# Kernel optimization log

Measured on AMD Instinct MI355X. Metric: run time of the kernel, lower is better.

The kernel has to match this reference:

```python
import jax, jax.numpy as jnp
import numpy as np

HEADS = 4
DIM_K = 16
DIM_U = 1
EPS = 1e-5


def _rel_pos_idx(n):
    # torch: meshgrid(ij) -> stack -> '(i j) n'; rel = pos[None,:]-pos[:,None] + n-1
    ii, jj = np.meshgrid(np.arange(n), np.arange(n), indexing='ij')
    pos = np.stack([ii, jj]).reshape(2, -1).T  # (n*n, 2)
    rel = pos[None, :] - pos[:, None] + (n - 1)  # (N, N, 2)
    return rel[..., 0], rel[..., 1]


def _bn(t, gamma, beta):
    # BatchNorm2d in training mode: batch stats over (b, h, w), biased var
    mu = t.mean(axis=(0, 1, 2))
    var = t.var(axis=(0, 1, 2))
    return (t - mu) * jax.lax.rsqrt(var + EPS) * gamma + beta


def setup_inputs() -> dict:
    key = jax.random.key(0)
    ks = jax.random.split(key, 16)
    b, n, c = 8, 48, 128
    hk = DIM_K * HEADS          # 64
    v = 128 // HEADS            # 32 (dim_out // heads)
    rl = 2 * n - 1              # 95
    s = 0.02
    return {
        'x': jax.random.normal(ks[0], (b, n, n, c), jnp.float32),
        'cor': jax.random.normal(ks[1], (b, n, n, 2), jnp.float32),
        'Wq': jax.random.normal(ks[2], (hk, c), jnp.float32) * s,
        'Wk': jax.random.normal(ks[3], (DIM_K * DIM_U, c), jnp.float32) * s,
        'Wv': jax.random.normal(ks[4], (v * DIM_U, c), jnp.float32) * s,
        'Wce': jax.random.normal(ks[5], (hk, 2), jnp.float32) * s,
        'bce': jax.random.normal(ks[6], (hk,), jnp.float32) * s,
        'Wcc': jax.random.normal(ks[7], (hk, 128), jnp.float32) * s,
        'Wmp': jax.random.normal(ks[8], (128, hk), jnp.float32) * s,
        'bmp': jax.random.normal(ks[9], (128,), jnp.float32) * s,
        'gq': jnp.ones((hk,), jnp.float32),
        'bq': jnp.zeros((hk,), jnp.float32),
        'gv': jnp.ones((v * DIM_U,), jnp.float32),
        'bv': jnp.zeros((v * DIM_U,), jnp.float32),
        'rel_pos_emb': jax.random.normal(ks[10], (rl, rl, DIM_K, DIM_U), jnp.float32),
    }


def reference(x, cor, Wq, Wk, Wv, Wce, bce, Wcc, Wmp, bmp, gq, bq, gv, bv, rel_pos_emb):
    b, hh, ww, c = x.shape
    h, u, kd = HEADS, DIM_U, DIM_K
    vd = Wv.shape[0] // u
    N = hh * ww

    # frame reversal along batch
    x_rev = jnp.concatenate([x[b // 2:], x[:b // 2]], axis=0)

    # 1x1 convs as channel matmuls (channels-last)
    q = jnp.einsum('bhwc,oc->bhwo', x, Wq)
    k = jnp.einsum('bhwc,oc->bhwo', x_rev, Wk)
    v = jnp.einsum('bhwc,oc->bhwo', x_rev, Wv)

    Qn = _bn(q, gq, bq)
    Vn = _bn(v, gv, bv)

    Q = jnp.transpose(Qn.reshape(b, N, h, kd), (0, 2, 3, 1))       # b h k n
    K = jnp.transpose(k.reshape(b, N, u, kd), (0, 2, 3, 1))        # b u k m
    V = jnp.transpose(Vn.reshape(b, N, u, vd), (0, 2, 3, 1))       # b u v m

    K = jax.nn.softmax(K, axis=-1)
    lamc = jnp.einsum('bukm,buvm->bkv', K, V)
    Yc = jnp.einsum('bhkn,bkv->bhvn', Q, lamc)

    # relative position lambda (global branch)
    ni, mi = _rel_pos_idx(hh)
    emb = rel_pos_emb[ni, mi]                                      # n m k u
    lamp = jnp.einsum('nmku,buvm->bnkv', emb, V)
    Yp = jnp.einsum('bhkn,bnkv->bhvn', Q, lamp)

    Y = Yc + Yp                                                    # b h v n
    appearance = jnp.transpose(Y.reshape(b, h, vd, hh, ww), (0, 3, 4, 1, 2)).reshape(b, hh, ww, h * vd)

    cor_embed_ = jnp.einsum('bhwc,oc->bhwo', cor, Wce) + bce       # b hh ww (h k)
    cor_embed = jnp.transpose(cor_embed_.reshape(b, N, h, kd), (0, 2, 3, 1))  # b h k n
    crc = jnp.einsum('bhkn,bkv->bhvn', cor_embed, lamc)
    crp = jnp.einsum('bhkn,bnkv->bhvn', cor_embed, lamp)
    cor_reverse_ = jnp.transpose((crc + crp).reshape(b, h, vd, hh, ww), (0, 3, 4, 1, 2)).reshape(b, hh, ww, h * vd)
    cor_reverse = jnp.einsum('bhwc,oc->bhwo', cor_reverse_, Wcc)
    motion = jnp.einsum('bhwc,oc->bhwo', cor_reverse - cor_embed_, Wmp) + bmp
    return appearance, motion
```

## Files before the change

### kernel.cpp

```cpp
#include <hip/hip_runtime.h>
#include <math.h>

#define NNPOS 2304
#define ROWS  18432
#define NK    96

#define O_Q   0ul
#define O_K   1179648ul
#define O_V   1474560ul
#define O_ST  2064384ul
#define O_VP  2064704ul
#define O_QP  2457920ul
#define O_CE  4817216ul
#define O_LC  5996864ul
#define O_CR  6000960ul
#define O_RT  8360256ul
#define O_WF  8433984ul
#define O_WG  8450368ul
#define O_B2  8450624ul
#define O_WB  8450752ul

typedef __bf16 bf16x8 __attribute__((ext_vector_type(8)));
typedef float  f32x4  __attribute__((ext_vector_type(4)));
typedef unsigned int u32;
typedef u32 u32x4 __attribute__((ext_vector_type(4)));

__device__ inline float wred(float v) {
#pragma unroll
  for (int off = 32; off > 0; off >>= 1) v += __shfl_down(v, off, 64);
  return v;
}

__global__ void k_fold(const float* __restrict__ Wcc, const float* __restrict__ Wce,
                       const float* __restrict__ Wmp, const float* __restrict__ bmp,
                       const float* __restrict__ bce, const float* __restrict__ Wq,
                       const float* __restrict__ Wk, const float* __restrict__ Wv,
                       float* __restrict__ ws) {
  const int t = threadIdx.x;
  const int g = blockIdx.x * 256 + t;
  const int o2 = g >> 7, c = g & 127;
  float acc = 0.f;
#pragma unroll 8
  for (int o = 0; o < 64; ++o) acc += Wmp[o2 * 64 + o] * Wcc[o * 128 + c];
  ws[O_WF + (size_t)c * 128 + o2] = acc;
  if (blockIdx.x == 0 && t < 128) {
    float a0 = 0.f, a1 = 0.f, ab = 0.f;
#pragma unroll 8
    for (int o = 0; o < 64; ++o) {
      float w = Wmp[t * 64 + o];
      a0 += w * Wce[o * 2]; a1 += w * Wce[o * 2 + 1]; ab += w * bce[o];
    }
    ws[O_WG + t * 2] = a0; ws[O_WG + t * 2 + 1] = a1; ws[O_B2 + t] = bmp[t] - ab;
  }
  __bf16* wbp = (__bf16*)(ws + O_WB);
  if (g < 14336) {
    float w;
    if (g < 8192) w = Wq[g];
    else if (g < 10240) w = Wk[g - 8192];
    else w = Wv[g - 10240];
    wbp[g] = (__bf16)w;
  }
}

__global__ __launch_bounds__(256) void k_qkv(const float* __restrict__ x,
                                             float* __restrict__ ws) {
  const int t = threadIdx.x;
  const int wave = t >> 6, lane = t & 63;
  const int lr = lane & 15, quad = lane >> 4;
  const int r0 = blockIdx.x * 64 + wave * 16;
  const int b = r0 / NNPOS;
  const int n0 = r0 - b * NNPOS;
  const size_t outbase = (size_t)(((b + 4) & 7)) * NNPOS + n0;

  const __bf16* wb = (const __bf16*)(ws + O_WB);
  const float* xrow = x + (size_t)(r0 + lr) * 128;

  f32x4 acc[7];
#pragma unroll
  for (int i = 0; i < 7; ++i) acc[i] = (f32x4){0.f, 0.f, 0.f, 0.f};

#pragma unroll
  for (int ks = 0; ks < 4; ++ks) {
    const float* ap = xrow + ks * 32 + quad * 8;
    float4 a0 = *(const float4*)(ap);
    float4 a1 = *(const float4*)(ap + 4);
    bf16x8 af;
    af[0] = (__bf16)a0.x; af[1] = (__bf16)a0.y; af[2] = (__bf16)a0.z; af[3] = (__bf16)a0.w;
    af[4] = (__bf16)a1.x; af[5] = (__bf16)a1.y; af[6] = (__bf16)a1.z; af[7] = (__bf16)a1.w;
#pragma unroll
    for (int ct = 0; ct < 7; ++ct) {
      bf16x8 bfrag = *(const bf16x8*)(wb + (ct * 16 + lr) * 128 + ks * 32 + quad * 8);
      acc[ct] = __builtin_amdgcn_mfma_f32_16x16x32_bf16(af, bfrag, acc[ct], 0, 0, 0);
    }
  }

#pragma unroll
  for (int ct = 0; ct < 7; ++ct) {
#pragma unroll
    for (int reg = 0; reg < 4; ++reg) {
      int m = quad * 4 + reg;
      int oc = ct * 16 + lr;
      float vvv = acc[ct][reg];
      if (ct < 4)      ws[O_Q + (size_t)(r0 + m) * 64 + oc] = vvv;
      else if (ct < 5) ws[O_K + (outbase + m) * 16 + (oc - 64)] = vvv;
      else             ws[O_V + (outbase + m) * 32 + (oc - 80)] = vvv;
    }
  }
}

__global__ void k_rt(const float* __restrict__ rel, float* __restrict__ ws) {
  __bf16* rt = (__bf16*)(ws + O_RT);
  int i = blockIdx.x * 256 + threadIdx.x;
  if (i < 144400) {
    int kc = i & 15, rr = i >> 4;
    int ri = rr / 95, rj = rr - ri * 95;
    rt[(size_t)kc * 9216 + ri * 96 + rj] = (__bf16)rel[i];
  }
}

__global__ void k_zero(float* __restrict__ ws) {
  __bf16* vp = (__bf16*)(ws + O_VP);
  int i = blockIdx.x * 256 + threadIdx.x;
  int bv = i / 96, rem = i - bv * 96;
  int mi = rem >> 1, h8 = rem & 1;
  uint4 z; z.x = 0; z.y = 0; z.z = 0; z.w = 0;
  *(uint4*)(vp + (size_t)bv * 3072 + mi * 64 + 48 + h8 * 8) = z;
}

__global__ void k_stats(const float* __restrict__ gq, const float* __restrict__ bq,
                        const float* __restrict__ gv, const float* __restrict__ bv,
                        float* __restrict__ ws) {
  const int t = threadIdx.x, blk = blockIdx.x;
  const int wave = t >> 6, lane = t & 63;
  __shared__ float r1[4], r2[4];
  if (blk < 96) {
    const bool isq = blk < 64;
    const int ch = isq ? blk : blk - 64;
    const float* src = ws + (isq ? O_Q : O_V);
    const int stride = isq ? 64 : 32;
    float s = 0.f, s2 = 0.f;
    for (int r = t; r < ROWS; r += 256) {
      float v = src[(size_t)r * stride + ch];
      s += v; s2 += v * v;
    }
    s = wred(s); s2 = wred(s2);
    if (lane == 0) { r1[wave] = s; r2[wave] = s2; }
    __syncthreads();
    if (t == 0) {
      float S = r1[0] + r1[1] + r1[2] + r1[3];
      float S2 = r2[0] + r2[1] + r2[2] + r2[3];
      float mu = S / 18432.f;
      float var = S2 / 18432.f - mu * mu;
      float g = isq ? gq[ch] : gv[ch];
      float be = isq ? bq[ch] : bv[ch];
      float sc = g * rsqrtf(var + 1e-5f);
      if (isq) { ws[O_ST + ch] = sc;       ws[O_ST + 64 + ch] = be - mu * sc; }
      else     { ws[O_ST + 128 + ch] = sc; ws[O_ST + 160 + ch] = be - mu * sc; }
    }
  } else {
    const int idx = blk - 96;
    const int b = idx >> 4, kc = idx & 15;
    float s = 0.f;
    for (int m = t; m < NNPOS; m += 256)
      s += __expf(ws[O_K + (size_t)(b * NNPOS + m) * 16 + kc]);
    s = wred(s);
    if (lane == 0) r1[wave] = s;
    __syncthreads();
    if (t == 0) ws[O_ST + 192 + idx] = 1.f / (r1[0] + r1[1] + r1[2] + r1[3]);
  }
}

__global__ void k_prep(const float* __restrict__ cor, const float* __restrict__ Wce,
                       const float* __restrict__ bce, float* __restrict__ ws) {
  const int t = threadIdx.x;
  const int rl = t >> 5, j = t & 31;
  const int rid = blockIdx.x * 8 + rl;
  const int b = rid / NNPOS, n = rid - b * NNPOS;
  const float* st = ws + O_ST;
  __bf16* vp = (__bf16*)(ws + O_VP);
  float vvn = ws[O_V + (size_t)rid * 32 + j] * st[128 + j] + st[160 + j];
  vp[(size_t)(b * 32 + j) * 3072 + (n / 48) * 64 + (n % 48)] = (__bf16)vvn;
  float c0 = cor[rid * 2], c1 = cor[rid * 2 + 1];
#pragma unroll
  for (int ch = j; ch < 64; ch += 32) {
    float qn = ws[O_Q + (size_t)rid * 64 + ch] * st[ch] + st[64 + ch];
    ws[O_QP + (size_t)(n * 8 + b) * 128 + ch] = qn;
    float ce = c0 * Wce[ch * 2] + c1 * Wce[ch * 2 + 1] + bce[ch];
    ws[O_QP + (size_t)(n * 8 + b) * 128 + 64 + ch] = ce;
    ws[O_CE + (size_t)rid * 64 + ch] = ce;
  }
}

__global__ void k_lamc(float* __restrict__ ws) {
  const int b = blockIdx.x >> 4, kc = blockIdx.x & 15;
  const int v = threadIdx.x & 31, chunk = threadIdx.x >> 5;
  const float* st = ws + O_ST;
  const float sc = st[128 + v], bi = st[160 + v];
  float acc = 0.f;
  const int mbeg = chunk * 288;
  for (int m = mbeg; m < mbeg + 288; ++m) {
    float ek = __expf(ws[O_K + (size_t)(b * NNPOS + m) * 16 + kc]);
    float vn = ws[O_V + (size_t)(b * NNPOS + m) * 32 + v] * sc + bi;
    acc += ek * vn;
  }
  __shared__ float red[8][32];
  red[chunk][v] = acc;
  __syncthreads();
  if (chunk == 0) {
    float s = 0.f;
#pragma unroll
    for (int q = 0; q < 8; ++q) s += red[q][v];
    ws[O_LC + (size_t)(b * 16 + kc) * 32 + v] = s * st[192 + b * 16 + kc];
  }
}

__global__ __launch_bounds__(256, 2) void k_lamp(float* __restrict__ ws,
                                                 float* __restrict__ out) {
  __shared__ __align__(16) char smem[33792];
  bf16x8* Bs16 = (bf16x8*)smem;
  u32* Sw = (u32*)(smem + 8192);
  float* Cs = (float*)smem;

  const int t = threadIdx.x;
  const int bx = blockIdx.x;
  const int ni = bx / 6;
  const int sset = bx - ni * 6;
  const int s0 = (sset < 3) ? sset * 16 : (sset - 3) * 16 + 1;
  const int chalf = blockIdx.y;
  const int colbase = chalf * 128;
  const int wave = t >> 6, lane = t & 63;
  const int wrow = wave >> 1, wcol = wave & 1;
  const int lr = lane & 15, quad = lane >> 4;

  const __bf16* vp = (const __bf16*)(ws + O_VP);
  const unsigned short* rp = (const unsigned short*)(ws + O_RT);

  const int ia0 = t;
  const int kcA0 = ia0 / 24, wpA0 = ia0 - kcA0 * 24;
  const int ia1 = t + 256;
  const int kcA1 = ia1 / 24, wpA1 = ia1 - kcA1 * 24;
  const bool hasA1 = (ia1 < 384);

  const int colB0 = t >> 2, pB0 = ((t & 3) - ((t >> 3) & 3)) & 3;
  const int ub1 = t + 256;
  const int colB1 = ub1 >> 2, pB1 = ((ub1 & 3) - ((ub1 >> 3) & 3)) & 3;
  const __bf16* gB0 = vp + (size_t)(colbase + colB0) * 3072 + pB0 * 8;
  const __bf16* gB1 = vp + (size_t)(colbase + colB1) * 3072 + pB1 * 8;

  f32x4 acc[4][4];
  {
    f32x4 zz = {0.f, 0.f, 0.f, 0.f};
#pragma unroll
    for (int i = 0; i < 4; ++i)
#pragma unroll
      for (int j = 0; j < 4; ++j) acc[i][j] = zz;
  }

  u32 sa0 = 0, sa1 = 0;
  bf16x8 vb0, vb1;

  {
    const int P0 = 96 * (47 - ni) - s0 + 33;
    long b0 = (long)kcA0 * 9216 + P0 + 2 * wpA0;
    if (P0 & 1) sa0 = (u32)rp[b0] | ((u32)rp[b0 + 1] << 16);
    else        sa0 = *(const u32*)(rp + b0);
    if (hasA1) {
      long b1 = (long)kcA1 * 9216 + P0 + 2 * wpA1;
      if (P0 & 1) sa1 = (u32)rp[b1] | ((u32)rp[b1 + 1] << 16);
      else        sa1 = *(const u32*)(rp + b1);
    }
    vb0 = *(const bf16x8*)(gB0);
    vb1 = *(const bf16x8*)(gB1);
  }

  for (int ks = 0; ks < NK; ++ks) {
    __syncthreads();
    Sw[kcA0 * 25 + wpA0] = sa0;
    if (hasA1) Sw[kcA1 * 25 + wpA1] = sa1;
    Bs16[t] = vb0;
    Bs16[t + 256] = vb1;
    __syncthreads();

    if (ks < NK - 1) {
      const int ksn = ks + 1;
      const int mi = ksn >> 1, mj0 = (ksn & 1) << 5;
      const int P0 = 96 * (mi - ni + 47) + mj0 - s0 + 33;
      const int k0 = ksn * 32;
      long b0 = (long)kcA0 * 9216 + P0 + 2 * wpA0;
      if (P0 & 1) sa0 = (u32)rp[b0] | ((u32)rp[b0 + 1] << 16);
      else        sa0 = *(const u32*)(rp + b0);
      if (hasA1) {
        long b1 = (long)kcA1 * 9216 + P0 + 2 * wpA1;
        if (P0 & 1) sa1 = (u32)rp[b1] | ((u32)rp[b1 + 1] << 16);
        else        sa1 = *(const u32*)(rp + b1);
      }
      vb0 = *(const bf16x8*)(gB0 + k0);
      vb1 = *(const bf16x8*)(gB1 + k0);
    }

    bf16x8 af[4], bfr[4];
#pragma unroll
    for (int rt = 0; rt < 4; ++rt) {
      int nl = wrow * 4 + rt;
      int wb = lr * 25 + (7 - nl) + quad * 4;
      u32x4 dd = { Sw[wb], Sw[wb + 1], Sw[wb + 2], Sw[wb + 3] };
      af[rt] = __builtin_bit_cast(bf16x8, dd);
    }
#pragma unroll
    for (int ct = 0; ct < 4; ++ct) {
      int col = wcol * 64 + ct * 16 + lr;
      int u = col * 4 + ((quad + (col >> 1)) & 3);
      bfr[ct] = Bs16[u];
    }
#pragma unroll
    for (int rt = 0; rt < 4; ++rt)
#pragma unroll
      for (int ct = 0; ct < 4; ++ct)
        acc[rt][ct] = __builtin_amdgcn_mfma_f32_16x16x32_bf16(af[rt], bfr[ct], acc[rt][ct], 0, 0, 0);
  }

  const float* lamc = ws + O_LC;
  const float* Qp = ws + O_QP;
  float* CR = ws + O_CR;
  const int s = t >> 5, vv = t & 31;

  for (int h = 0; h < 2; ++h) {
    __syncthreads();
    if (wrow == h) {
#pragma unroll
      for (int rt = 0; rt < 4; ++rt) {
#pragma unroll
        for (int ct = 0; ct < 4; ++ct) {
          int col = wcol * 64 + ct * 16 + lr;
          int bb = chalf * 4 + (col >> 5);
          int vl = col & 31;
#pragma unroll
          for (int reg = 0; reg < 4; ++reg) {
            int row = rt * 16 + quad * 4 + reg;
            int kc = row & 15;
            Cs[row * 132 + col] = acc[rt][ct][reg] + lamc[(bb * 16 + kc) * 32 + vl];
          }
        }
      }
    }
    __syncthreads();
#pragma unroll
    for (int i = 0; i < 16; ++i) {
      int combo = s * 16 + i;
      int hp = combo & 7, bl = (combo >> 3) & 3, nr = combo >> 5;
      int n = ni * 48 + s0 + 2 * (h * 4 + nr);
      int bb = chalf * 4 + bl;
      const float* qrow = Qp + ((size_t)(n * 8 + bb) * 8 + hp) * 16;
      const float* crow = Cs + (nr * 16) * 132 + bl * 32 + vv;
      float y = 0.f;
#pragma unroll
      for (int kc = 0; kc < 16; ++kc) y += qrow[kc] * crow[kc * 132];
      float* dst = (hp < 4) ? out : CR;
      dst[(size_t)(bb * NNPOS + n) * 128 + (hp & 3) * 32 + vv] = y;
    }
  }
}

__global__ void k_motion(const float* __restrict__ cor, float* __restrict__ ws,
                         float* __restrict__ out) {
  __shared__ float cr[16][128];
  __shared__ float cc[16][2];
  const int t = threadIdx.x;
  const int r0 = blockIdx.x * 16;
  for (int i = t; i < 2048; i += 256) cr[i >> 7][i & 127] = ws[O_CR + (size_t)r0 * 128 + i];
  if (t < 32) cc[t >> 1][t & 1] = cor[r0 * 2 + t];
  __syncthreads();
  const int o2 = t & 127, rg = t >> 7;
  const float* wft = ws + O_WF;
  float wg0 = ws[O_WG + o2 * 2], wg1 = ws[O_WG + o2 * 2 + 1], b2 = ws[O_B2 + o2];
  float acc[8];
#pragma unroll
  for (int j = 0; j < 8; ++j) {
    int row = rg + 2 * j;
    acc[j] = b2 - cc[row][0] * wg0 - cc[row][1] * wg1;
  }
  for (int c = 0; c < 128; ++c) {
    float w = wft[c * 128 + o2];
#pragma unroll
    for (int j = 0; j < 8; ++j) acc[j] += cr[rg + 2 * j][c] * w;
  }
#pragma unroll
  for (int j = 0; j < 8; ++j)
    out[2359296ul + (size_t)(r0 + rg + 2 * j) * 128 + o2] = acc[j];
}

extern "C" void kernel_launch(void* const* d_in, const int* in_sizes, int n_in,
                              void* d_out, int out_size, void* d_ws, size_t ws_size,
                              hipStream_t stream) {
  const float* x   = (const float*)d_in[0];
  const float* cor = (const float*)d_in[1];
  const float* Wq  = (const float*)d_in[2];
  const float* Wk  = (const float*)d_in[3];
  const float* Wv  = (const float*)d_in[4];
  const float* Wce = (const float*)d_in[5];
  const float* bce = (const float*)d_in[6];
  const float* Wcc = (const float*)d_in[7];
  const float* Wmp = (const float*)d_in[8];
  const float* bmp = (const float*)d_in[9];
  const float* gq  = (const float*)d_in[10];
  const float* bq  = (const float*)d_in[11];
  const float* gv  = (const float*)d_in[12];
  const float* bv  = (const float*)d_in[13];
  const float* rel = (const float*)d_in[14];
  float* out = (float*)d_out;
  float* ws  = (float*)d_ws;

  k_fold  <<<64, 256, 0, stream>>>(Wcc, Wce, Wmp, bmp, bce, Wq, Wk, Wv, ws);
  k_qkv   <<<288, 256, 0, stream>>>(x, ws);
  k_rt    <<<565, 256, 0, stream>>>(rel, ws);
  k_zero  <<<96, 256, 0, stream>>>(ws);
  k_stats <<<224, 256, 0, stream>>>(gq, bq, gv, bv, ws);
  k_prep  <<<2304, 256, 0, stream>>>(cor, Wce, bce, ws);
  k_lamc  <<<128, 256, 0, stream>>>(ws);
  k_lamp  <<<dim3(288, 2), 256, 0, stream>>>(ws, out);
  k_motion<<<1152, 256, 0, stream>>>(cor, ws, out);
}
```

Baseline: 267.7 us.

## Use MFMA for motion GEMM, split stats reductions, double-buffer lamp loads

The motion projection now runs as a bf16 MFMA GEMM, with the folded weight and the cor_reverse intermediate stored in bf16, replacing the scalar fp32 loop. The BN and softmax-sum statistics become a two-stage reduction: many coalesced partial-sum blocks, then one finalizing block. k_lamc is tiled through shared memory and accumulates with atomics, with the softmax normalization deferred to k_lamp. k_lamp's global loads are double-buffered two steps ahead, and the redundant CE store is dropped. The bf16 intermediates lower precision, and the extra launch and atomics add a little overhead.

```diff
diff --git a/kernel.cpp b/kernel.cpp
--- a/kernel.cpp
+++ b/kernel.cpp
@@ -15,21 +15,18 @@
 #define O_LC  5996864ul
 #define O_CR  6000960ul
 #define O_RT  8360256ul
-#define O_WF  8433984ul
 #define O_WG  8450368ul
 #define O_B2  8450624ul
 #define O_WB  8450752ul
+#define O_PT  8457920ul
+#define O_PV  8466112ul
+#define O_PE  8468160ul
+#define O_WFB 8469184ul
 
 typedef __bf16 bf16x8 __attribute__((ext_vector_type(8)));
 typedef float  f32x4  __attribute__((ext_vector_type(4)));
 typedef unsigned int u32;
 typedef u32 u32x4 __attribute__((ext_vector_type(4)));
-
-__device__ inline float wred(float v) {
-#pragma unroll
-  for (int off = 32; off > 0; off >>= 1) v += __shfl_down(v, off, 64);
-  return v;
-}
 
 __global__ void k_fold(const float* __restrict__ Wcc, const float* __restrict__ Wce,
                        const float* __restrict__ Wmp, const float* __restrict__ bmp,
@@ -42,7 +39,7 @@
   float acc = 0.f;
 #pragma unroll 8
   for (int o = 0; o < 64; ++o) acc += Wmp[o2 * 64 + o] * Wcc[o * 128 + c];
-  ws[O_WF + (size_t)c * 128 + o2] = acc;
+  ((__bf16*)(ws + O_WFB))[o2 * 128 + c] = (__bf16)acc;
   if (blockIdx.x == 0 && t < 128) {
     float a0 = 0.f, a1 = 0.f, ab = 0.f;
 #pragma unroll 8
@@ -121,52 +118,95 @@
 __global__ void k_zero(float* __restrict__ ws) {
   __bf16* vp = (__bf16*)(ws + O_VP);
   int i = blockIdx.x * 256 + threadIdx.x;
+  if (i < 4096) ws[O_LC + i] = 0.f;
   int bv = i / 96, rem = i - bv * 96;
   int mi = rem >> 1, h8 = rem & 1;
   uint4 z; z.x = 0; z.y = 0; z.z = 0; z.w = 0;
   *(uint4*)(vp + (size_t)bv * 3072 + mi * 64 + 48 + h8 * 8) = z;
 }
 
-__global__ void k_stats(const float* __restrict__ gq, const float* __restrict__ bq,
-                        const float* __restrict__ gv, const float* __restrict__ bv,
-                        float* __restrict__ ws) {
+__global__ void k_stats1(float* __restrict__ ws) {
   const int t = threadIdx.x, blk = blockIdx.x;
-  const int wave = t >> 6, lane = t & 63;
-  __shared__ float r1[4], r2[4];
-  if (blk < 96) {
-    const bool isq = blk < 64;
-    const int ch = isq ? blk : blk - 64;
-    const float* src = ws + (isq ? O_Q : O_V);
-    const int stride = isq ? 64 : 32;
+  __shared__ float sh[512];
+  if (blk < 64) {
+    const int ch = t & 63, rsub = t >> 6;
+    const float* src = ws + O_Q;
+    const int r0 = blk * 288;
     float s = 0.f, s2 = 0.f;
-    for (int r = t; r < ROWS; r += 256) {
-      float v = src[(size_t)r * stride + ch];
+#pragma unroll 4
+    for (int i = 0; i < 72; ++i) {
+      float v = src[(size_t)(r0 + rsub + i * 4) * 64 + ch];
       s += v; s2 += v * v;
     }
-    s = wred(s); s2 = wred(s2);
-    if (lane == 0) { r1[wave] = s; r2[wave] = s2; }
-    __syncthreads();
-    if (t == 0) {
-      float S = r1[0] + r1[1] + r1[2] + r1[3];
-      float S2 = r2[0] + r2[1] + r2[2] + r2[3];
-      float mu = S / 18432.f;
-      float var = S2 / 18432.f - mu * mu;
-      float g = isq ? gq[ch] : gv[ch];
-      float be = isq ? bq[ch] : bv[ch];
-      float sc = g * rsqrtf(var + 1e-5f);
-      if (isq) { ws[O_ST + ch] = sc;       ws[O_ST + 64 + ch] = be - mu * sc; }
-      else     { ws[O_ST + 128 + ch] = sc; ws[O_ST + 160 + ch] = be - mu * sc; }
+    sh[t] = s; sh[256 + t] = s2;
+    __syncthreads();
+    if (t < 64) {
+      float S = sh[t] + sh[t + 64] + sh[t + 128] + sh[t + 192];
+      float S2 = sh[256 + t] + sh[256 + t + 64] + sh[256 + t + 128] + sh[256 + t + 192];
+      ws[O_PT + blk * 128 + t * 2] = S; ws[O_PT + blk * 128 + t * 2 + 1] = S2;
+    }
+  } else if (blk < 96) {
+    const int j = blk - 64;
+    const int ch = t & 31, rsub = t >> 5;
+    const float* src = ws + O_V;
+    const int r0 = j * 576;
+    float s = 0.f, s2 = 0.f;
+#pragma unroll 4
+    for (int i = 0; i < 72; ++i) {
+      float v = src[(size_t)(r0 + rsub + i * 8) * 32 + ch];
+      s += v; s2 += v * v;
+    }
+    sh[t] = s; sh[256 + t] = s2;
+    __syncthreads();
+    if (t < 32) {
+      float S = 0.f, S2 = 0.f;
+#pragma unroll
+      for (int k = 0; k < 8; ++k) { S += sh[t + k * 32]; S2 += sh[256 + t + k * 32]; }
+      ws[O_PV + j * 64 + t * 2] = S; ws[O_PV + j * 64 + t * 2 + 1] = S2;
     }
   } else {
     const int idx = blk - 96;
-    const int b = idx >> 4, kc = idx & 15;
+    const int b = idx >> 3, sl = idx & 7;
+    const int kc = t & 15, rsub = t >> 4;
+    const int r0 = b * 2304 + sl * 288;
     float s = 0.f;
-    for (int m = t; m < NNPOS; m += 256)
-      s += __expf(ws[O_K + (size_t)(b * NNPOS + m) * 16 + kc]);
-    s = wred(s);
-    if (lane == 0) r1[wave] = s;
-    __syncthreads();
-    if (t == 0) ws[O_ST + 192 + idx] = 1.f / (r1[0] + r1[1] + r1[2] + r1[3]);
+#pragma unroll 2
+    for (int i = 0; i < 18; ++i)
+      s += __expf(ws[O_K + (size_t)(r0 + rsub + i * 16) * 16 + kc]);
+    sh[t] = s;
+    __syncthreads();
+    if (t < 16) {
+      float S = 0.f;
+#pragma unroll
+      for (int k = 0; k < 16; ++k) S += sh[t + k * 16];
+      ws[O_PE + b * 128 + sl * 16 + t] = S;
+    }
+  }
+}
+
+__global__ void k_stats2(const float* __restrict__ gq, const float* __restrict__ bq,
+                         const float* __restrict__ gv, const float* __restrict__ bv,
+                         float* __restrict__ ws) {
+  const int t = threadIdx.x;
+  if (t < 64) {
+    float S = 0.f, S2 = 0.f;
+    for (int i = 0; i < 64; ++i) { S += ws[O_PT + i * 128 + t * 2]; S2 += ws[O_PT + i * 128 + t * 2 + 1]; }
+    float mu = S / 18432.f, var = S2 / 18432.f - mu * mu;
+    float sc = gq[t] * rsqrtf(var + 1e-5f);
+    ws[O_ST + t] = sc; ws[O_ST + 64 + t] = bq[t] - mu * sc;
+  } else if (t < 96) {
+    int ch = t - 64;
+    float S = 0.f, S2 = 0.f;
+    for (int i = 0; i < 32; ++i) { S += ws[O_PV + i * 64 + ch * 2]; S2 += ws[O_PV + i * 64 + ch * 2 + 1]; }
+    float mu = S / 18432.f, var = S2 / 18432.f - mu * mu;
+    float sc = gv[ch] * rsqrtf(var + 1e-5f);
+    ws[O_ST + 128 + ch] = sc; ws[O_ST + 160 + ch] = bv[ch] - mu * sc;
+  } else if (t < 224) {
+    int idx = t - 96; int b = idx >> 4, kc = idx & 15;
+    float S = 0.f;
+#pragma unroll
+    for (int sl = 0; sl < 8; ++sl) S += ws[O_PE + b * 128 + sl * 16 + kc];
+    ws[O_ST + 192 + idx] = 1.f / S;
   }
 }
 
@@ -187,31 +227,37 @@
     ws[O_QP + (size_t)(n * 8 + b) * 128 + ch] = qn;
     float ce = c0 * Wce[ch * 2] + c1 * Wce[ch * 2 + 1] + bce[ch];
     ws[O_QP + (size_t)(n * 8 + b) * 128 + 64 + ch] = ce;
-    ws[O_CE + (size_t)rid * 64 + ch] = ce;
   }
 }
 
 __global__ void k_lamc(float* __restrict__ ws) {
-  const int b = blockIdx.x >> 4, kc = blockIdx.x & 15;
-  const int v = threadIdx.x & 31, chunk = threadIdx.x >> 5;
+  const int b = blockIdx.x / 9, sl = blockIdx.x - b * 9;
+  const int t = threadIdx.x;
+  __shared__ float eK[16][16];
+  __shared__ float Vn[16][33];
   const float* st = ws + O_ST;
-  const float sc = st[128 + v], bi = st[160 + v];
-  float acc = 0.f;
-  const int mbeg = chunk * 288;
-  for (int m = mbeg; m < mbeg + 288; ++m) {
-    float ek = __expf(ws[O_K + (size_t)(b * NNPOS + m) * 16 + kc]);
-    float vn = ws[O_V + (size_t)(b * NNPOS + m) * 32 + v] * sc + bi;
-    acc += ek * vn;
-  }
-  __shared__ float red[8][32];
-  red[chunk][v] = acc;
-  __syncthreads();
-  if (chunk == 0) {
-    float s = 0.f;
-#pragma unroll
-    for (int q = 0; q < 8; ++q) s += red[q][v];
-    ws[O_LC + (size_t)(b * 16 + kc) * 32 + v] = s * st[192 + b * 16 + kc];
-  }
+  const int kc = t & 15, vp_ = t >> 4;
+  const int v0 = vp_ * 2, v1 = v0 + 1;
+  float a0 = 0.f, a1 = 0.f;
+  const int m0 = b * 2304 + sl * 256;
+  const int jj = t & 31, rw = t >> 5;
+  const float scj = st[128 + jj], bij = st[160 + jj];
+  for (int ch = 0; ch < 16; ++ch) {
+    const int mbase = m0 + ch * 16;
+    eK[t >> 4][t & 15] = __expf(ws[O_K + (size_t)(mbase + (t >> 4)) * 16 + (t & 15)]);
+    Vn[rw][jj]     = ws[O_V + (size_t)(mbase + rw) * 32 + jj] * scj + bij;
+    Vn[rw + 8][jj] = ws[O_V + (size_t)(mbase + rw + 8) * 32 + jj] * scj + bij;
+    __syncthreads();
+#pragma unroll
+    for (int m = 0; m < 16; ++m) {
+      float e = eK[m][kc];
+      a0 += e * Vn[m][v0];
+      a1 += e * Vn[m][v1];
+    }
+    __syncthreads();
+  }
+  atomicAdd(&ws[O_LC + (size_t)(b * 16 + kc) * 32 + v0], a0);
+  atomicAdd(&ws[O_LC + (size_t)(b * 16 + kc) * 32 + v1], a1);
 }
 
 __global__ __launch_bounds__(256, 2) void k_lamp(float* __restrict__ ws,
@@ -256,47 +302,36 @@
       for (int j = 0; j < 4; ++j) acc[i][j] = zz;
   }
 
-  u32 sa0 = 0, sa1 = 0;
-  bf16x8 vb0, vb1;
-
-  {
-    const int P0 = 96 * (47 - ni) - s0 + 33;
+  u32 sa[2] = {0, 0}, sb[2] = {0, 0};
+  bf16x8 vA[2], vB[2];
+
+  auto loadStep = [&](int ksn, u32& sA_, u32& sB_, bf16x8& v0_, bf16x8& v1_) {
+    const int mi = ksn >> 1, mj0 = (ksn & 1) << 5;
+    const int P0 = 96 * (mi - ni + 47) + mj0 - s0 + 33;
+    const int k0 = ksn * 32;
     long b0 = (long)kcA0 * 9216 + P0 + 2 * wpA0;
-    if (P0 & 1) sa0 = (u32)rp[b0] | ((u32)rp[b0 + 1] << 16);
-    else        sa0 = *(const u32*)(rp + b0);
+    if (P0 & 1) sA_ = (u32)rp[b0] | ((u32)rp[b0 + 1] << 16);
+    else        sA_ = *(const u32*)(rp + b0);
     if (hasA1) {
       long b1 = (long)kcA1 * 9216 + P0 + 2 * wpA1;
-      if (P0 & 1) sa1 = (u32)rp[b1] | ((u32)rp[b1 + 1] << 16);
-      else        sa1 = *(const u32*)(rp + b1);
-    }
-    vb0 = *(const bf16x8*)(gB0);
-    vb1 = *(const bf16x8*)(gB1);
-  }
-
-  for (int ks = 0; ks < NK; ++ks) {
-    __syncthreads();
-    Sw[kcA0 * 25 + wpA0] = sa0;
-    if (hasA1) Sw[kcA1 * 25 + wpA1] = sa1;
-    Bs16[t] = vb0;
-    Bs16[t + 256] = vb1;
-    __syncthreads();
-
-    if (ks < NK - 1) {
-      const int ksn = ks + 1;
-      const int mi = ksn >> 1, mj0 = (ksn & 1) << 5;
-      const int P0 = 96 * (mi - ni + 47) + mj0 - s0 + 33;
-      const int k0 = ksn * 32;
-      long b0 = (long)kcA0 * 9216 + P0 + 2 * wpA0;
-      if (P0 & 1) sa0 = (u32)rp[b0] | ((u32)rp[b0 + 1] << 16);
-      else        sa0 = *(const u32*)(rp + b0);
-      if (hasA1) {
-        long b1 = (long)kcA1 * 9216 + P0 + 2 * wpA1;
-        if (P0 & 1) sa1 = (u32)rp[b1] | ((u32)rp[b1 + 1] << 16);
-        else        sa1 = *(const u32*)(rp + b1);
-      }
-      vb0 = *(const bf16x8*)(gB0 + k0);
-      vb1 = *(const bf16x8*)(gB1 + k0);
-    }
+      if (P0 & 1) sB_ = (u32)rp[b1] | ((u32)rp[b1 + 1] << 16);
+      else        sB_ = *(const u32*)(rp + b1);
+    }
+    v0_ = *(const bf16x8*)(gB0 + k0);
+    v1_ = *(const bf16x8*)(gB1 + k0);
+  };
+
+  loadStep(0, sa[0], sb[0], vA[0], vB[0]);
+  loadStep(1, sa[1], sb[1], vA[1], vB[1]);
+
+  auto step = [&](int ks, u32& sA_, u32& sB_, bf16x8& v0_, bf16x8& v1_) {
+    __syncthreads();
+    Sw[kcA0 * 25 + wpA0] = sA_;
+    if (hasA1) Sw[kcA1 * 25 + wpA1] = sB_;
+    Bs16[t] = v0_;
+    Bs16[t + 256] = v1_;
+    __syncthreads();
+    if (ks + 2 < NK) loadStep(ks + 2, sA_, sB_, v0_, v1_);
 
     bf16x8 af[4], bfr[4];
 #pragma unroll
@@ -317,11 +352,16 @@
 #pragma unroll
       for (int ct = 0; ct < 4; ++ct)
         acc[rt][ct] = __builtin_amdgcn_mfma_f32_16x16x32_bf16(af[rt], bfr[ct], acc[rt][ct], 0, 0, 0);
+  };
+
+  for (int ks2 = 0; ks2 < NK; ks2 += 2) {
+    step(ks2,     sa[0], sb[0], vA[0], vB[0]);
+    step(ks2 + 1, sa[1], sb[1], vA[1], vB[1]);
   }
 
   const float* lamc = ws + O_LC;
   const float* Qp = ws + O_QP;
-  float* CR = ws + O_CR;
+  __bf16* CRb = (__bf16*)(ws + O_CR);
   const int s = t >> 5, vv = t & 31;
 
   for (int h = 0; h < 2; ++h) {
@@ -338,7 +378,8 @@
           for (int reg = 0; reg < 4; ++reg) {
             int row = rt * 16 + quad * 4 + reg;
             int kc = row & 15;
-            Cs[row * 132 + col] = acc[rt][ct][reg] + lamc[(bb * 16 + kc) * 32 + vl];
+            float dinv = ws[O_ST + 192 + bb * 16 + kc];
+            Cs[row * 132 + col] = acc[rt][ct][reg] + lamc[(bb * 16 + kc) * 32 + vl] * dinv;
           }
         }
       }
@@ -355,38 +396,48 @@
       float y = 0.f;
 #pragma unroll
       for (int kc = 0; kc < 16; ++kc) y += qrow[kc] * crow[kc * 132];
-      float* dst = (hp < 4) ? out : CR;
-      dst[(size_t)(bb * NNPOS + n) * 128 + (hp & 3) * 32 + vv] = y;
-    }
-  }
-}
-
-__global__ void k_motion(const float* __restrict__ cor, float* __restrict__ ws,
-                         float* __restrict__ out) {
-  __shared__ float cr[16][128];
-  __shared__ float cc[16][2];
-  const int t = threadIdx.x;
-  const int r0 = blockIdx.x * 16;
-  for (int i = t; i < 2048; i += 256) cr[i >> 7][i & 127] = ws[O_CR + (size_t)r0 * 128 + i];
-  if (t < 32) cc[t >> 1][t & 1] = cor[r0 * 2 + t];
-  __syncthreads();
-  const int o2 = t & 127, rg = t >> 7;
-  const float* wft = ws + O_WF;
-  float wg0 = ws[O_WG + o2 * 2], wg1 = ws[O_WG + o2 * 2 + 1], b2 = ws[O_B2 + o2];
-  float acc[8];
-#pragma unroll
-  for (int j = 0; j < 8; ++j) {
-    int row = rg + 2 * j;
-    acc[j] = b2 - cc[row][0] * wg0 - cc[row][1] * wg1;
-  }
-  for (int c = 0; c < 128; ++c) {
-    float w = wft[c * 128 + o2];
-#pragma unroll
-    for (int j = 0; j < 8; ++j) acc[j] += cr[rg + 2 * j][c] * w;
-  }
-#pragma unroll
-  for (int j = 0; j < 8; ++j)
-    out[2359296ul + (size_t)(r0 + rg + 2 * j) * 128 + o2] = acc[j];
+      size_t idx = (size_t)(bb * NNPOS + n) * 128 + (hp & 3) * 32 + vv;
+      if (hp < 4) out[idx] = y;
+      else        CRb[idx] = (__bf16)y;
+    }
+  }
+}
+
+__global__ __launch_bounds__(256) void k_motion(const float* __restrict__ cor,
+                                                float* __restrict__ ws,
+                                                float* __restrict__ out) {
+  const int t = threadIdx.x;
+  const int wave = t >> 6, lane = t & 63;
+  const int lr = lane & 15, quad = lane >> 4;
+  const int r0 = blockIdx.x * 64 + wave * 16;
+  const __bf16* crb = (const __bf16*)(ws + O_CR);
+  const __bf16* wfb = (const __bf16*)(ws + O_WFB);
+
+  f32x4 acc[8];
+#pragma unroll
+  for (int i = 0; i < 8; ++i) acc[i] = (f32x4){0.f, 0.f, 0.f, 0.f};
+
+#pragma unroll
+  for (int ks = 0; ks < 4; ++ks) {
+    bf16x8 af = *(const bf16x8*)(crb + (size_t)(r0 + lr) * 128 + ks * 32 + quad * 8);
+#pragma unroll
+    for (int ct = 0; ct < 8; ++ct) {
+      bf16x8 bfrag = *(const bf16x8*)(wfb + (ct * 16 + lr) * 128 + ks * 32 + quad * 8);
+      acc[ct] = __builtin_amdgcn_mfma_f32_16x16x32_bf16(af, bfrag, acc[ct], 0, 0, 0);
+    }
+  }
+
+#pragma unroll
+  for (int reg = 0; reg < 4; ++reg) {
+    int row = r0 + quad * 4 + reg;
+    float c0 = cor[row * 2], c1 = cor[row * 2 + 1];
+#pragma unroll
+    for (int ct = 0; ct < 8; ++ct) {
+      int o2 = ct * 16 + lr;
+      float y = acc[ct][reg] + ws[O_B2 + o2] - c0 * ws[O_WG + o2 * 2] - c1 * ws[O_WG + o2 * 2 + 1];
+      out[2359296ul + (size_t)row * 128 + o2] = y;
+    }
+  }
 }
 
 extern "C" void kernel_launch(void* const* d_in, const int* in_sizes, int n_in,
@@ -414,9 +465,10 @@
   k_qkv   <<<288, 256, 0, stream>>>(x, ws);
   k_rt    <<<565, 256, 0, stream>>>(rel, ws);
   k_zero  <<<96, 256, 0, stream>>>(ws);
-  k_stats <<<224, 256, 0, stream>>>(gq, bq, gv, bv, ws);
+  k_stats1<<<160, 256, 0, stream>>>(ws);
+  k_stats2<<<1, 256, 0, stream>>>(gq, bq, gv, bv, ws);
+  k_lamc  <<<72, 256, 0, stream>>>(ws);
   k_prep  <<<2304, 256, 0, stream>>>(cor, Wce, bce, ws);
-  k_lamc  <<<128, 256, 0, stream>>>(ws);
   k_lamp  <<<dim3(288, 2), 256, 0, stream>>>(ws, out);
-  k_motion<<<1152, 256, 0, stream>>>(cor, ws, out);
-}
+  k_motion<<<288, 256, 0, stream>>>(cor, ws, out);
+}
```

New measurement: 261.2 us. 2.4% less time.
